# Kernel tuning notes

Hardware: AMD Instinct MI355X
Metric: run time of the kernel (lower is better)

Reference implementation:

```python
import jax, jax.numpy as jnp
import numpy as np

N_NODES = 100000
N_EDGES = 1600000
N_GRAPHS = 64
IN_CH = 128
HIDDEN = 128
OUT_CH = 2


def gcn_conv(x, row, col, W, b, num_nodes):
    # PyG GCNConv: add self-loops, symmetric deg^{-1/2} normalization,
    # linear transform, scatter-add aggregation, then bias.
    loop = jnp.arange(num_nodes, dtype=row.dtype)
    r = jnp.concatenate([row, loop])  # source nodes
    c = jnp.concatenate([col, loop])  # target nodes
    deg = jax.ops.segment_sum(jnp.ones_like(c, dtype=x.dtype), c, num_segments=num_nodes)
    dinv = jnp.where(deg > 0, jax.lax.rsqrt(deg), 0.0)
    norm = dinv[r] * dinv[c]  # [E+N]
    h = x @ W  # [N, F_out]
    msg = norm[:, None] * h[r]  # gather [E+N, F_out]
    agg = jax.ops.segment_sum(msg, c, num_segments=num_nodes)  # scatter-add
    return agg + b


def setup_inputs() -> dict:
    key = jax.random.key(0)
    ks = jax.random.split(key, 8)
    x = jax.random.normal(ks[0], (N_NODES, IN_CH), dtype=jnp.float32)
    edge_index = jax.random.randint(ks[1], (2, N_EDGES), 0, N_NODES, dtype=jnp.int32)
    batch = jnp.sort(jax.random.randint(ks[2], (N_NODES,), 0, N_GRAPHS, dtype=jnp.int32))
    s1 = 1.0 / np.sqrt(IN_CH)
    s2 = 1.0 / np.sqrt(HIDDEN)
    W1 = jax.random.normal(ks[3], (IN_CH, HIDDEN), dtype=jnp.float32) * s1
    b1 = jnp.zeros((HIDDEN,), dtype=jnp.float32)
    W2 = jax.random.normal(ks[4], (HIDDEN, HIDDEN), dtype=jnp.float32) * s2
    b2 = jnp.zeros((HIDDEN,), dtype=jnp.float32)
    Wlin = jax.random.normal(ks[5], (HIDDEN, OUT_CH), dtype=jnp.float32) * s2
    blin = jnp.zeros((OUT_CH,), dtype=jnp.float32)
    return {"x": x, "edge_index": edge_index, "batch": batch,
            "W1": W1, "b1": b1, "W2": W2, "b2": b2, "Wlin": Wlin, "blin": blin}


def reference(x, edge_index, batch, W1, b1, W2, b2, Wlin, blin):
    row, col = edge_index[0], edge_index[1]
    h = jax.nn.relu(gcn_conv(x, row, col, W1, b1, N_NODES))
    h = jax.nn.relu(gcn_conv(h, row, col, W2, b2, N_NODES))
    # global_mean_pool over graph ids
    sums = jax.ops.segment_sum(h, batch, num_segments=N_GRAPHS)  # [G, H]
    cnts = jax.ops.segment_sum(jnp.ones((h.shape[0],), dtype=h.dtype), batch, num_segments=N_GRAPHS)
    pooled = sums / jnp.maximum(cnts, 1.0)[:, None]
    return pooled @ Wlin + blin  # [G, OUT_CH]
```

## Files before the change

kernel.cpp:

```cpp
#include <hip/hip_runtime.h>
#include <hip/hip_bf16.h>
#include <hip/hip_fp16.h>

#define N_NODES  100000
#define N_EDGES  1600000
#define N_GRAPHS 64

#define NB       256
#define BSZ      391
#define NE4      (N_EDGES/4)
#define NBLK     391
#define ROWMASK  0x1FFFF

typedef __attribute__((ext_vector_type(4))) float    f32x4;
typedef __attribute__((ext_vector_type(8))) _Float16 f16x8;

__global__ __launch_bounds__(256) void sortcount_kernel(const int4* __restrict__ col4,
                                                        int* __restrict__ blockcnt) {
    __shared__ int hist[NB];
    int t = threadIdx.x, blk = blockIdx.x;
    hist[t] = 0;
    __syncthreads();
#pragma unroll
    for (int j = 0; j < 4; ++j) {
        int i = blk * 1024 + j * 256 + t;
        if (i < NE4) {
            int4 c = col4[i];
            atomicAdd(&hist[c.x / BSZ], 1);
            atomicAdd(&hist[c.y / BSZ], 1);
            atomicAdd(&hist[c.z / BSZ], 1);
            atomicAdd(&hist[c.w / BSZ], 1);
        }
    }
    __syncthreads();
    blockcnt[blk * NB + t] = hist[t];
}

__global__ __launch_bounds__(256) void sortscan_kernel(int* __restrict__ blockcnt,
                                                       int* __restrict__ buckettotal) {
    int b = blockIdx.x, t = threadIdx.x;
    __shared__ int sc[256];
    int e0 = 2 * t, e1 = 2 * t + 1;
    int v0 = (e0 < NBLK) ? blockcnt[e0 * NB + b] : 0;
    int v1 = (e1 < NBLK) ? blockcnt[e1 * NB + b] : 0;
    int ps = v0 + v1;
    sc[t] = ps;
    __syncthreads();
    for (int d = 1; d < 256; d <<= 1) {
        int x = (t >= d) ? sc[t - d] : 0;
        __syncthreads();
        sc[t] += x;
        __syncthreads();
    }
    int ex = sc[t] - ps;
    if (e0 < NBLK) blockcnt[e0 * NB + b] = ex;
    if (e1 < NBLK) blockcnt[e1 * NB + b] = ex + v0;
    if (t == 255) buckettotal[b] = sc[255];
}

__global__ __launch_bounds__(256) void sortbase_kernel(const int* __restrict__ buckettotal,
                                                       int* __restrict__ bucket_base,
                                                       int* __restrict__ off) {
    __shared__ int sc[256];
    int t = threadIdx.x;
    int v = buckettotal[t];
    sc[t] = v;
    __syncthreads();
    for (int d = 1; d < 256; d <<= 1) {
        int x = (t >= d) ? sc[t - d] : 0;
        __syncthreads();
        sc[t] += x;
        __syncthreads();
    }
    bucket_base[t] = sc[t] - v;
    if (t == 255) {
        bucket_base[256] = sc[255];
        off[N_NODES] = N_EDGES;
    }
}

__global__ __launch_bounds__(256) void sortscatter_kernel(const int4* __restrict__ row4,
                                                          const int4* __restrict__ col4,
                                                          const int* __restrict__ blockpre,
                                                          const int* __restrict__ bucket_base,
                                                          int* __restrict__ pairs) {
    __shared__ int cur[NB];
    int t = threadIdx.x, blk = blockIdx.x;
    cur[t] = bucket_base[t] + blockpre[blk * NB + t];
    __syncthreads();
#pragma unroll
    for (int j = 0; j < 4; ++j) {
        int i = blk * 1024 + j * 256 + t;
        if (i < NE4) {
            int4 r = row4[i];
            int4 c = col4[i];
            int b0 = c.x / BSZ, b1 = c.y / BSZ, b2 = c.z / BSZ, b3 = c.w / BSZ;
            int p0 = atomicAdd(&cur[b0], 1); pairs[p0] = ((c.x - b0 * BSZ) << 17) | r.x;
            int p1 = atomicAdd(&cur[b1], 1); pairs[p1] = ((c.y - b1 * BSZ) << 17) | r.y;
            int p2 = atomicAdd(&cur[b2], 1); pairs[p2] = ((c.z - b2 * BSZ) << 17) | r.z;
            int p3 = atomicAdd(&cur[b3], 1); pairs[p3] = ((c.w - b3 * BSZ) << 17) | r.w;
        }
    }
}

__global__ __launch_bounds__(256) void sortlocal_kernel(const int* __restrict__ pairs,
                                                        const int* __restrict__ bucket_base,
                                                        const int* __restrict__ buckettotal,
                                                        int* __restrict__ sortr,
                                                        int* __restrict__ off,
                                                        float* __restrict__ dinv) {
    int b = blockIdx.x, t = threadIdx.x;
    int base = bucket_base[b];
    int cnt  = buckettotal[b];
    int c0   = b * BSZ;
    int nc   = N_NODES - c0; if (nc > BSZ) nc = BSZ;

    __shared__ int hist[BSZ];
    __shared__ int sc[256];
    for (int i = t; i < nc; i += 256) hist[i] = 0;
    __syncthreads();
    for (int i = t; i < cnt; i += 256) {
        int pc = pairs[base + i];
        atomicAdd(&hist[pc >> 17], 1);
    }
    __syncthreads();
    int e0 = 2 * t, e1 = 2 * t + 1;
    int h0 = (e0 < nc) ? hist[e0] : 0;
    int h1 = (e1 < nc) ? hist[e1] : 0;
    int ps = h0 + h1;
    sc[t] = ps;
    __syncthreads();
    for (int d = 1; d < 256; d <<= 1) {
        int x = (t >= d) ? sc[t - d] : 0;
        __syncthreads();
        sc[t] += x;
        __syncthreads();
    }
    int ex = sc[t] - ps;
    if (e0 < nc) { off[c0 + e0] = base + ex;      dinv[c0 + e0] = rsqrtf((float)h0 + 1.f); }
    if (e1 < nc) { off[c0 + e1] = base + ex + h0; dinv[c0 + e1] = rsqrtf((float)h1 + 1.f); }
    __syncthreads();
    if (e0 < nc) hist[e0] = base + ex;
    if (e1 < nc) hist[e1] = base + ex + h0;
    __syncthreads();
    for (int i = t; i < cnt; i += 256) {
        int pc = pairs[base + i];
        int pos = atomicAdd(&hist[pc >> 17], 1);
        sortr[pos] = pc & ROWMASK;
    }
}

__global__ __launch_bounds__(256) void wpack_zero_kernel(const float* __restrict__ W1,
                                                         const float* __restrict__ W2,
                                                         _Float16* __restrict__ Wp1,
                                                         _Float16* __restrict__ Wp2,
                                                         float* __restrict__ pooled,
                                                         float* __restrict__ gcnt) {
    int tid = blockIdx.x * 256 + threadIdx.x;
    for (int i = tid; i < N_GRAPHS * 128 + N_GRAPHS; i += 4096) {
        if (i < N_GRAPHS * 128) pooled[i] = 0.f;
        else gcnt[i - N_GRAPHS * 128] = 0.f;
    }
    const float* W = (tid < 2048) ? W1 : W2;
    _Float16*   Wp = (tid < 2048) ? Wp1 : Wp2;
    int t = tid & 2047;
    int f = t >> 6, lane = t & 63;
    int j = f >> 2, s = f & 3;
    int kb = s * 32 + (lane >> 4) * 8;
    int c  = j * 16 + (lane & 15);
#pragma unroll
    for (int i = 0; i < 8; ++i)
        Wp[(size_t)t * 8 + i] = (_Float16)W[(kb + i) * 128 + c];
}

__global__ __launch_bounds__(256) void gemm_mfma_kernel(const float* __restrict__ X,
                                                        const _Float16* __restrict__ Wp,
                                                        const float* __restrict__ dinv,
                                                        _Float16* __restrict__ out) {
    __shared__ _Float16 Wl[16384];
    {
        const float4* src = (const float4*)Wp;
        float4* dst = (float4*)Wl;
        for (int i = threadIdx.x; i < 2048; i += 256) dst[i] = src[i];
    }
    __syncthreads();

    int wv = threadIdx.x >> 6, lane = threadIdx.x & 63;
    int tile = blockIdx.x * 4 + wv;
    if (tile >= N_NODES / 16) return;
    int n0 = tile * 16;
    int m = lane & 15, b = lane >> 4;

    f16x8 a[4];
    const float* base = X + (size_t)(n0 + m) * 128 + b * 8;
#pragma unroll
    for (int s = 0; s < 4; ++s) {
        float4 u = *(const float4*)(base + s * 32);
        float4 v = *(const float4*)(base + s * 32 + 4);
        f16x8 tt;
        tt[0] = (_Float16)u.x; tt[1] = (_Float16)u.y;
        tt[2] = (_Float16)u.z; tt[3] = (_Float16)u.w;
        tt[4] = (_Float16)v.x; tt[5] = (_Float16)v.y;
        tt[6] = (_Float16)v.z; tt[7] = (_Float16)v.w;
        a[s] = tt;
    }

    f32x4 acc[8];
#pragma unroll
    for (int j = 0; j < 8; ++j) acc[j] = (f32x4){0.f, 0.f, 0.f, 0.f};
#pragma unroll
    for (int j = 0; j < 8; ++j)
#pragma unroll
        for (int s = 0; s < 4; ++s) {
            f16x8 bf = *(const f16x8*)&Wl[(j * 4 + s) * 512 + lane * 8];
            acc[j] = __builtin_amdgcn_mfma_f32_16x16x32_f16(a[s], bf, acc[j], 0, 0, 0);
        }

    float dv0 = dinv[n0 + b * 4 + 0];
    float dv1 = dinv[n0 + b * 4 + 1];
    float dv2 = dinv[n0 + b * 4 + 2];
    float dv3 = dinv[n0 + b * 4 + 3];
#pragma unroll
    for (int j = 0; j < 8; ++j) {
        _Float16* o = out + (size_t)(n0 + b * 4) * 128 + j * 16 + m;
        o[0 * 128] = (_Float16)(acc[j][0] * dv0);
        o[1 * 128] = (_Float16)(acc[j][1] * dv1);
        o[2 * 128] = (_Float16)(acc[j][2] * dv2);
        o[3 * 128] = (_Float16)(acc[j][3] * dv3);
    }
}

__device__ __forceinline__ float2 gather_row(const __half* __restrict__ hs,
                                             const int* __restrict__ sortr,
                                             int c, int e0, int e1, long chb) {
    float2 s = __half22float2(*(const __half2*)&hs[(long)c * 128 + chb]);
    float a0x = s.x, a0y = s.y;
    float a1x = 0.f, a1y = 0.f, a2x = 0.f, a2y = 0.f, a3x = 0.f, a3y = 0.f;
    int e = e0;
    for (; e + 4 <= e1; e += 4) {
        int r0 = sortr[e + 0], r1 = sortr[e + 1];
        int r2 = sortr[e + 2], r3 = sortr[e + 3];
        float2 v0 = __half22float2(*(const __half2*)&hs[(long)r0 * 128 + chb]);
        float2 v1 = __half22float2(*(const __half2*)&hs[(long)r1 * 128 + chb]);
        float2 v2 = __half22float2(*(const __half2*)&hs[(long)r2 * 128 + chb]);
        float2 v3 = __half22float2(*(const __half2*)&hs[(long)r3 * 128 + chb]);
        a0x += v0.x; a0y += v0.y;
        a1x += v1.x; a1y += v1.y;
        a2x += v2.x; a2y += v2.y;
        a3x += v3.x; a3y += v3.y;
    }
    for (; e < e1; ++e) {
        int r0 = sortr[e];
        float2 v0 = __half22float2(*(const __half2*)&hs[(long)r0 * 128 + chb]);
        a0x += v0.x; a0y += v0.y;
    }
    float2 r;
    r.x = (a0x + a1x) + (a2x + a3x);
    r.y = (a0y + a1y) + (a2y + a3y);
    return r;
}

__global__ __launch_bounds__(256) void agg_gemm_kernel(const __half* __restrict__ hs,
                                                       const int* __restrict__ sortr,
                                                       const int* __restrict__ off,
                                                       const float* __restrict__ dinv,
                                                       const float* __restrict__ bias,
                                                       const _Float16* __restrict__ Wp,
                                                       _Float16* __restrict__ out) {
    __shared__ float rowbuf[16 * 132];
    int t = threadIdx.x;
    int wv = t >> 6, lane = t & 63;
    int c0 = blockIdx.x * 16;
    const long chb = 2 * (long)lane;
    float2 bb = *(const float2*)&bias[chb];

#pragma unroll
    for (int i = 0; i < 4; ++i) {
        int c = c0 + wv * 4 + i;
        float2 g = gather_row(hs, sortr, c, off[c], off[c + 1], chb);
        float dv = dinv[c];
        float rx = fmaxf(fmaf(g.x, dv, bb.x), 0.f);
        float ry = fmaxf(fmaf(g.y, dv, bb.y), 0.f);
        rowbuf[(wv * 4 + i) * 132 + 2 * lane]     = rx;
        rowbuf[(wv * 4 + i) * 132 + 2 * lane + 1] = ry;
    }
    __syncthreads();

    int m = lane & 15, b = lane >> 4;
    f16x8 a[4];
#pragma unroll
    for (int s = 0; s < 4; ++s) {
        const float* rb = &rowbuf[m * 132 + s * 32 + b * 8];
        float4 u = *(const float4*)rb;
        float4 v = *(const float4*)(rb + 4);
        f16x8 tt;
        tt[0] = (_Float16)u.x; tt[1] = (_Float16)u.y;
        tt[2] = (_Float16)u.z; tt[3] = (_Float16)u.w;
        tt[4] = (_Float16)v.x; tt[5] = (_Float16)v.y;
        tt[6] = (_Float16)v.z; tt[7] = (_Float16)v.w;
        a[s] = tt;
    }

    f32x4 acc[2];
    acc[0] = (f32x4){0.f, 0.f, 0.f, 0.f};
    acc[1] = (f32x4){0.f, 0.f, 0.f, 0.f};
#pragma unroll
    for (int jj = 0; jj < 2; ++jj) {
        int j = wv * 2 + jj;
#pragma unroll
        for (int s = 0; s < 4; ++s) {
            f16x8 bf = *(const f16x8*)&Wp[((size_t)(j * 4 + s) * 64 + lane) * 8];
            acc[jj] = __builtin_amdgcn_mfma_f32_16x16x32_f16(a[s], bf, acc[jj], 0, 0, 0);
        }
    }

    float dv0 = dinv[c0 + b * 4 + 0];
    float dv1 = dinv[c0 + b * 4 + 1];
    float dv2 = dinv[c0 + b * 4 + 2];
    float dv3 = dinv[c0 + b * 4 + 3];
#pragma unroll
    for (int jj = 0; jj < 2; ++jj) {
        int j = wv * 2 + jj;
        _Float16* o = out + (size_t)(c0 + b * 4) * 128 + j * 16 + m;
        o[0 * 128] = (_Float16)(acc[jj][0] * dv0);
        o[1 * 128] = (_Float16)(acc[jj][1] * dv1);
        o[2 * 128] = (_Float16)(acc[jj][2] * dv2);
        o[3 * 128] = (_Float16)(acc[jj][3] * dv3);
    }
}

__global__ __launch_bounds__(256) void agg_pool_kernel(const __half* __restrict__ hs2,
                                                       const int* __restrict__ sortr,
                                                       const int* __restrict__ off,
                                                       const float* __restrict__ dinv,
                                                       const float* __restrict__ bias,
                                                       const int* __restrict__ batch,
                                                       float* __restrict__ pooled,
                                                       float* __restrict__ gcnt) {
    __shared__ float redA[4][128];
    __shared__ float redB[4][128];
    int t = threadIdx.x;
    int wv = t >> 6, lane = t & 63;
    int c0 = blockIdx.x * 16;
    const long chb = 2 * (long)lane;
    float2 bb = *(const float2*)&bias[chb];

    int g0   = batch[c0];
    int gend = batch[c0 + 15];
    bool slow = (gend > g0 + 1);

    float2 accA = make_float2(0.f, 0.f);
    float2 accB = make_float2(0.f, 0.f);

#pragma unroll
    for (int i = 0; i < 4; ++i) {
        int c = c0 + wv * 4 + i;
        float2 g = gather_row(hs2, sortr, c, off[c], off[c + 1], chb);
        float dv = dinv[c];
        float rx = fmaxf(fmaf(g.x, dv, bb.x), 0.f);
        float ry = fmaxf(fmaf(g.y, dv, bb.y), 0.f);
        int gg = batch[c];
        if (!slow) {
            if (gg == g0) { accA.x += rx; accA.y += ry; }
            else          { accB.x += rx; accB.y += ry; }
        } else {
            atomicAdd(&pooled[(size_t)gg * 128 + chb],     rx);
            atomicAdd(&pooled[(size_t)gg * 128 + chb + 1], ry);
        }
    }

    if (!slow) {
        redA[wv][2 * lane]     = accA.x;
        redA[wv][2 * lane + 1] = accA.y;
        redB[wv][2 * lane]     = accB.x;
        redB[wv][2 * lane + 1] = accB.y;
        __syncthreads();
        if (wv == 0) {
            int ch0 = 2 * lane, ch1 = 2 * lane + 1;
            float sA0 = (redA[0][ch0] + redA[1][ch0]) + (redA[2][ch0] + redA[3][ch0]);
            float sA1 = (redA[0][ch1] + redA[1][ch1]) + (redA[2][ch1] + redA[3][ch1]);
            atomicAdd(&pooled[(size_t)g0 * 128 + ch0], sA0);
            atomicAdd(&pooled[(size_t)g0 * 128 + ch1], sA1);
            if (gend != g0) {
                float sB0 = (redB[0][ch0] + redB[1][ch0]) + (redB[2][ch0] + redB[3][ch0]);
                float sB1 = (redB[0][ch1] + redB[1][ch1]) + (redB[2][ch1] + redB[3][ch1]);
                atomicAdd(&pooled[(size_t)gend * 128 + ch0], sB0);
                atomicAdd(&pooled[(size_t)gend * 128 + ch1], sB1);
            }
        }
        if (t == 0) {
            int nB = 0;
#pragma unroll
            for (int k = 0; k < 16; ++k) nB += (batch[c0 + k] != g0) ? 1 : 0;
            atomicAdd(&gcnt[g0], (float)(16 - nB));
            if (nB) atomicAdd(&gcnt[gend], (float)nB);
        }
    } else {
        if (t == 0)
            for (int k = 0; k < 16; ++k) atomicAdd(&gcnt[batch[c0 + k]], 1.f);
    }
}

__global__ void final_kernel(const float* __restrict__ pooled,
                             const float* __restrict__ gcnt,
                             const float* __restrict__ Wlin,
                             const float* __restrict__ blin,
                             float* __restrict__ out) {
    int t = threadIdx.x;
    if (t >= N_GRAPHS * 2) return;
    int g = t >> 1, o = t & 1;
    float c = gcnt[g];
    if (c < 1.f) c = 1.f;
    float s = 0.f;
    for (int k = 0; k < 128; ++k)
        s += (pooled[g * 128 + k] / c) * Wlin[k * 2 + o];
    out[g * 2 + o] = s + blin[o];
}

extern "C" void kernel_launch(void* const* d_in, const int* in_sizes, int n_in,
                              void* d_out, int out_size, void* d_ws, size_t ws_size,
                              hipStream_t stream) {
    const float* x     = (const float*)d_in[0];
    const int*   row   = (const int*)d_in[1];
    const int*   col   = row + N_EDGES;
    const int*   batch = (const int*)d_in[2];
    const float* W1    = (const float*)d_in[3];
    const float* b1    = (const float*)d_in[4];
    const float* W2    = (const float*)d_in[5];
    const float* b2    = (const float*)d_in[6];
    const float* Wlin  = (const float*)d_in[7];
    const float* blin  = (const float*)d_in[8];
    float* out = (float*)d_out;

    char* w = (char*)d_ws;
    size_t p = 0;
    auto alloc = [&](size_t bytes) -> void* {
        void* r = w + p;
        p += (bytes + 511) & ~(size_t)511;
        return r;
    };
    int*      off         = (int*)alloc((size_t)(N_NODES + 1) * 4);
    float*    dinv        = (float*)alloc((size_t)N_NODES * 4);
    int*      sortr       = (int*)alloc((size_t)N_EDGES * 4);
    int*      pairs       = (int*)alloc((size_t)N_EDGES * 4);
    int*      blockcnt    = (int*)alloc((size_t)NBLK * NB * 4);
    int*      buckettotal = (int*)alloc((size_t)NB * 4);
    int*      bucket_base = (int*)alloc((size_t)(NB + 1) * 4);
    _Float16* Wp1         = (_Float16*)alloc((size_t)128 * 128 * 2);
    _Float16* Wp2         = (_Float16*)alloc((size_t)128 * 128 * 2);
    __half*   hs          = (__half*)alloc((size_t)N_NODES * 128 * 2);
    __half*   hs2         = (__half*)alloc((size_t)N_NODES * 128 * 2);
    float*    pooled      = (float*)alloc((size_t)N_GRAPHS * 128 * 4);
    float*    gcnt        = (float*)alloc((size_t)N_GRAPHS * 4);
    (void)ws_size; (void)in_sizes; (void)n_in; (void)out_size;

    sortcount_kernel<<<NBLK, 256, 0, stream>>>((const int4*)col, blockcnt);
    sortscan_kernel<<<NB, 256, 0, stream>>>(blockcnt, buckettotal);
    sortbase_kernel<<<1, 256, 0, stream>>>(buckettotal, bucket_base, off);
    sortscatter_kernel<<<NBLK, 256, 0, stream>>>((const int4*)row, (const int4*)col,
                                                 blockcnt, bucket_base, pairs);
    sortlocal_kernel<<<NB, 256, 0, stream>>>(pairs, bucket_base, buckettotal,
                                             sortr, off, dinv);
    wpack_zero_kernel<<<16, 256, 0, stream>>>(W1, W2, Wp1, Wp2, pooled, gcnt);

    gemm_mfma_kernel<<<(N_NODES / 16 + 3) / 4, 256, 0, stream>>>(x, Wp1, dinv, (_Float16*)hs);
    agg_gemm_kernel<<<N_NODES / 16, 256, 0, stream>>>(hs, sortr, off, dinv, b1, Wp2,
                                                      (_Float16*)hs2);
    agg_pool_kernel<<<N_NODES / 16, 256, 0, stream>>>(hs2, sortr, off, dinv, b2, batch,
                                                      pooled, gcnt);
    final_kernel<<<1, 128, 0, stream>>>(pooled, gcnt, Wlin, blin, out);
}
```

Measured before the change: 343.8 us.

## Use one wave per node in aggregation kernels with 1024-thread blocks

The two aggregation kernels now launch 1024 threads per block, so each of the 16 waves gathers one destination row instead of four waves gathering four rows each. This exposes more independent gathers in flight to hide memory latency. In agg_gemm only 8 of the 16 waves do the MFMA stage, one output column tile each. The pooling kernel moves its per-graph reduction into shared memory, where 128 threads sum the 16 rows per channel before the atomics. The cost is larger blocks with idle waves during the GEMM and reduction phases, plus register limits from the 1024-thread launch bounds.

```diff
diff --git a/kernel.cpp b/kernel.cpp
--- a/kernel.cpp
+++ b/kernel.cpp
@@ -260,13 +260,13 @@
     return r;
 }
 
-__global__ __launch_bounds__(256) void agg_gemm_kernel(const __half* __restrict__ hs,
-                                                       const int* __restrict__ sortr,
-                                                       const int* __restrict__ off,
-                                                       const float* __restrict__ dinv,
-                                                       const float* __restrict__ bias,
-                                                       const _Float16* __restrict__ Wp,
-                                                       _Float16* __restrict__ out) {
+__global__ __launch_bounds__(1024) void agg_gemm_kernel(const __half* __restrict__ hs,
+                                                        const int* __restrict__ sortr,
+                                                        const int* __restrict__ off,
+                                                        const float* __restrict__ dinv,
+                                                        const float* __restrict__ bias,
+                                                        const _Float16* __restrict__ Wp,
+                                                        _Float16* __restrict__ out) {
     __shared__ float rowbuf[16 * 132];
     int t = threadIdx.x;
     int wv = t >> 6, lane = t & 63;
@@ -274,130 +274,103 @@
     const long chb = 2 * (long)lane;
     float2 bb = *(const float2*)&bias[chb];
 
-#pragma unroll
-    for (int i = 0; i < 4; ++i) {
-        int c = c0 + wv * 4 + i;
+    {
+        int c = c0 + wv;
         float2 g = gather_row(hs, sortr, c, off[c], off[c + 1], chb);
         float dv = dinv[c];
-        float rx = fmaxf(fmaf(g.x, dv, bb.x), 0.f);
-        float ry = fmaxf(fmaf(g.y, dv, bb.y), 0.f);
-        rowbuf[(wv * 4 + i) * 132 + 2 * lane]     = rx;
-        rowbuf[(wv * 4 + i) * 132 + 2 * lane + 1] = ry;
-    }
-    __syncthreads();
-
-    int m = lane & 15, b = lane >> 4;
-    f16x8 a[4];
-#pragma unroll
-    for (int s = 0; s < 4; ++s) {
-        const float* rb = &rowbuf[m * 132 + s * 32 + b * 8];
-        float4 u = *(const float4*)rb;
-        float4 v = *(const float4*)(rb + 4);
-        f16x8 tt;
-        tt[0] = (_Float16)u.x; tt[1] = (_Float16)u.y;
-        tt[2] = (_Float16)u.z; tt[3] = (_Float16)u.w;
-        tt[4] = (_Float16)v.x; tt[5] = (_Float16)v.y;
-        tt[6] = (_Float16)v.z; tt[7] = (_Float16)v.w;
-        a[s] = tt;
-    }
-
-    f32x4 acc[2];
-    acc[0] = (f32x4){0.f, 0.f, 0.f, 0.f};
-    acc[1] = (f32x4){0.f, 0.f, 0.f, 0.f};
-#pragma unroll
-    for (int jj = 0; jj < 2; ++jj) {
-        int j = wv * 2 + jj;
+        rowbuf[wv * 132 + 2 * lane]     = fmaxf(fmaf(g.x, dv, bb.x), 0.f);
+        rowbuf[wv * 132 + 2 * lane + 1] = fmaxf(fmaf(g.y, dv, bb.y), 0.f);
+    }
+    __syncthreads();
+
+    if (wv < 8) {
+        int m = lane & 15, b = lane >> 4;
+        f16x8 a[4];
+#pragma unroll
+        for (int s = 0; s < 4; ++s) {
+            const float* rb = &rowbuf[m * 132 + s * 32 + b * 8];
+            float4 u = *(const float4*)rb;
+            float4 v = *(const float4*)(rb + 4);
+            f16x8 tt;
+            tt[0] = (_Float16)u.x; tt[1] = (_Float16)u.y;
+            tt[2] = (_Float16)u.z; tt[3] = (_Float16)u.w;
+            tt[4] = (_Float16)v.x; tt[5] = (_Float16)v.y;
+            tt[6] = (_Float16)v.z; tt[7] = (_Float16)v.w;
+            a[s] = tt;
+        }
+
+        f32x4 acc = (f32x4){0.f, 0.f, 0.f, 0.f};
+        const int j = wv;
 #pragma unroll
         for (int s = 0; s < 4; ++s) {
             f16x8 bf = *(const f16x8*)&Wp[((size_t)(j * 4 + s) * 64 + lane) * 8];
-            acc[jj] = __builtin_amdgcn_mfma_f32_16x16x32_f16(a[s], bf, acc[jj], 0, 0, 0);
-        }
-    }
-
-    float dv0 = dinv[c0 + b * 4 + 0];
-    float dv1 = dinv[c0 + b * 4 + 1];
-    float dv2 = dinv[c0 + b * 4 + 2];
-    float dv3 = dinv[c0 + b * 4 + 3];
-#pragma unroll
-    for (int jj = 0; jj < 2; ++jj) {
-        int j = wv * 2 + jj;
+            acc = __builtin_amdgcn_mfma_f32_16x16x32_f16(a[s], bf, acc, 0, 0, 0);
+        }
+
+        float dv0 = dinv[c0 + b * 4 + 0];
+        float dv1 = dinv[c0 + b * 4 + 1];
+        float dv2 = dinv[c0 + b * 4 + 2];
+        float dv3 = dinv[c0 + b * 4 + 3];
         _Float16* o = out + (size_t)(c0 + b * 4) * 128 + j * 16 + m;
-        o[0 * 128] = (_Float16)(acc[jj][0] * dv0);
-        o[1 * 128] = (_Float16)(acc[jj][1] * dv1);
-        o[2 * 128] = (_Float16)(acc[jj][2] * dv2);
-        o[3 * 128] = (_Float16)(acc[jj][3] * dv3);
-    }
-}
-
-__global__ __launch_bounds__(256) void agg_pool_kernel(const __half* __restrict__ hs2,
-                                                       const int* __restrict__ sortr,
-                                                       const int* __restrict__ off,
-                                                       const float* __restrict__ dinv,
-                                                       const float* __restrict__ bias,
-                                                       const int* __restrict__ batch,
-                                                       float* __restrict__ pooled,
-                                                       float* __restrict__ gcnt) {
-    __shared__ float redA[4][128];
-    __shared__ float redB[4][128];
+        o[0 * 128] = (_Float16)(acc[0] * dv0);
+        o[1 * 128] = (_Float16)(acc[1] * dv1);
+        o[2 * 128] = (_Float16)(acc[2] * dv2);
+        o[3 * 128] = (_Float16)(acc[3] * dv3);
+    }
+}
+
+__global__ __launch_bounds__(1024) void agg_pool_kernel(const __half* __restrict__ hs2,
+                                                        const int* __restrict__ sortr,
+                                                        const int* __restrict__ off,
+                                                        const float* __restrict__ dinv,
+                                                        const float* __restrict__ bias,
+                                                        const int* __restrict__ batch,
+                                                        float* __restrict__ pooled,
+                                                        float* __restrict__ gcnt) {
+    __shared__ float rowbuf[16 * 132];
+    __shared__ int gb[16];
     int t = threadIdx.x;
     int wv = t >> 6, lane = t & 63;
     int c0 = blockIdx.x * 16;
     const long chb = 2 * (long)lane;
     float2 bb = *(const float2*)&bias[chb];
 
-    int g0   = batch[c0];
-    int gend = batch[c0 + 15];
-    bool slow = (gend > g0 + 1);
-
-    float2 accA = make_float2(0.f, 0.f);
-    float2 accB = make_float2(0.f, 0.f);
-
-#pragma unroll
-    for (int i = 0; i < 4; ++i) {
-        int c = c0 + wv * 4 + i;
+    {
+        int c = c0 + wv;
         float2 g = gather_row(hs2, sortr, c, off[c], off[c + 1], chb);
         float dv = dinv[c];
-        float rx = fmaxf(fmaf(g.x, dv, bb.x), 0.f);
-        float ry = fmaxf(fmaf(g.y, dv, bb.y), 0.f);
-        int gg = batch[c];
+        rowbuf[wv * 132 + 2 * lane]     = fmaxf(fmaf(g.x, dv, bb.x), 0.f);
+        rowbuf[wv * 132 + 2 * lane + 1] = fmaxf(fmaf(g.y, dv, bb.y), 0.f);
+        if (lane == 0) gb[wv] = batch[c];
+    }
+    __syncthreads();
+
+    if (t < 128) {
+        int g0   = gb[0];
+        int gend = gb[15];
+        bool slow = (gend > g0 + 1);
         if (!slow) {
-            if (gg == g0) { accA.x += rx; accA.y += ry; }
-            else          { accB.x += rx; accB.y += ry; }
+            float sA = 0.f, sB = 0.f;
+#pragma unroll
+            for (int r = 0; r < 16; ++r) {
+                float v = rowbuf[r * 132 + t];
+                if (gb[r] == g0) sA += v; else sB += v;
+            }
+            atomicAdd(&pooled[(size_t)g0 * 128 + t], sA);
+            if (gend != g0) atomicAdd(&pooled[(size_t)gend * 128 + t], sB);
+            if (t == 0) {
+                int nA = 0;
+#pragma unroll
+                for (int r = 0; r < 16; ++r) nA += (gb[r] == g0) ? 1 : 0;
+                atomicAdd(&gcnt[g0], (float)nA);
+                if (gend != g0) atomicAdd(&gcnt[gend], (float)(16 - nA));
+            }
         } else {
-            atomicAdd(&pooled[(size_t)gg * 128 + chb],     rx);
-            atomicAdd(&pooled[(size_t)gg * 128 + chb + 1], ry);
-        }
-    }
-
-    if (!slow) {
-        redA[wv][2 * lane]     = accA.x;
-        redA[wv][2 * lane + 1] = accA.y;
-        redB[wv][2 * lane]     = accB.x;
-        redB[wv][2 * lane + 1] = accB.y;
-        __syncthreads();
-        if (wv == 0) {
-            int ch0 = 2 * lane, ch1 = 2 * lane + 1;
-            float sA0 = (redA[0][ch0] + redA[1][ch0]) + (redA[2][ch0] + redA[3][ch0]);
-            float sA1 = (redA[0][ch1] + redA[1][ch1]) + (redA[2][ch1] + redA[3][ch1]);
-            atomicAdd(&pooled[(size_t)g0 * 128 + ch0], sA0);
-            atomicAdd(&pooled[(size_t)g0 * 128 + ch1], sA1);
-            if (gend != g0) {
-                float sB0 = (redB[0][ch0] + redB[1][ch0]) + (redB[2][ch0] + redB[3][ch0]);
-                float sB1 = (redB[0][ch1] + redB[1][ch1]) + (redB[2][ch1] + redB[3][ch1]);
-                atomicAdd(&pooled[(size_t)gend * 128 + ch0], sB0);
-                atomicAdd(&pooled[(size_t)gend * 128 + ch1], sB1);
-            }
-        }
-        if (t == 0) {
-            int nB = 0;
-#pragma unroll
-            for (int k = 0; k < 16; ++k) nB += (batch[c0 + k] != g0) ? 1 : 0;
-            atomicAdd(&gcnt[g0], (float)(16 - nB));
-            if (nB) atomicAdd(&gcnt[gend], (float)nB);
-        }
-    } else {
-        if (t == 0)
-            for (int k = 0; k < 16; ++k) atomicAdd(&gcnt[batch[c0 + k]], 1.f);
+            for (int r = 0; r < 16; ++r)
+                atomicAdd(&pooled[(size_t)gb[r] * 128 + t], rowbuf[r * 132 + t]);
+            if (t == 0)
+                for (int r = 0; r < 16; ++r) atomicAdd(&gcnt[gb[r]], 1.f);
+        }
     }
 }
 
@@ -464,9 +437,9 @@
     wpack_zero_kernel<<<16, 256, 0, stream>>>(W1, W2, Wp1, Wp2, pooled, gcnt);
 
     gemm_mfma_kernel<<<(N_NODES / 16 + 3) / 4, 256, 0, stream>>>(x, Wp1, dinv, (_Float16*)hs);
-    agg_gemm_kernel<<<N_NODES / 16, 256, 0, stream>>>(hs, sortr, off, dinv, b1, Wp2,
-                                                      (_Float16*)hs2);
-    agg_pool_kernel<<<N_NODES / 16, 256, 0, stream>>>(hs2, sortr, off, dinv, b2, batch,
-                                                      pooled, gcnt);
+    agg_gemm_kernel<<<N_NODES / 16, 1024, 0, stream>>>(hs, sortr, off, dinv, b1, Wp2,
+                                                       (_Float16*)hs2);
+    agg_pool_kernel<<<N_NODES / 16, 1024, 0, stream>>>(hs2, sortr, off, dinv, b2, batch,
+                                                       pooled, gcnt);
     final_kernel<<<1, 128, 0, stream>>>(pooled, gcnt, Wlin, blin, out);
 }
```

Measured after the change: 353.2 us. 2.7% more time.
